# Performance work log

Measured on AMD Instinct MI355X. Metric: run time of the kernel, lower is better.

The kernel has to match this reference:

```python
import jax, jax.numpy as jnp
import numpy as np

N0, N1, N2 = 200000, 100000, 50000
E0, E1 = 1600000, 800000
IN_F, H_F, N_CLS = 128, 256, 64


def sage_conv(h_src, src_idx, dst_idx, num_dst, W_self, W_neigh, b):
    # DGL SAGEConv with aggregator_type='mean':
    #   h_neigh = mean over in-neighbors of h_src
    #   out = h_dst @ W_self + h_neigh @ W_neigh + b
    h_dst = h_src[:num_dst]
    msgs = h_src[src_idx]                                   # [E, F] gather
    summed = jax.ops.segment_sum(msgs, dst_idx, num_segments=num_dst)
    deg = jax.ops.segment_sum(jnp.ones((src_idx.shape[0],), h_src.dtype),
                              dst_idx, num_segments=num_dst)
    h_neigh = summed / jnp.maximum(deg, 1.0)[:, None]       # mean, safe for deg=0
    return h_dst @ W_self + h_neigh @ W_neigh + b


def setup_inputs() -> dict:
    key = jax.random.key(0)
    ks = jax.random.split(key, 10)
    s1 = 1.0 / np.sqrt(IN_F)
    s2 = 1.0 / np.sqrt(H_F)
    return {
        "x": jax.random.normal(ks[0], (N0, IN_F), jnp.float32),
        "src0": jax.random.randint(ks[1], (E0,), 0, N0, jnp.int64 if jax.config.jax_enable_x64 else jnp.int32),
        "dst0": jnp.sort(jax.random.randint(ks[2], (E0,), 0, N1)),
        "src1": jax.random.randint(ks[3], (E1,), 0, N1),
        "dst1": jnp.sort(jax.random.randint(ks[4], (E1,), 0, N2)),
        "num_dst0": N1,
        "num_dst1": N2,
        "W_self1": jax.random.normal(ks[5], (IN_F, H_F), jnp.float32) * s1,
        "W_neigh1": jax.random.normal(ks[6], (IN_F, H_F), jnp.float32) * s1,
        "b1": jnp.zeros((H_F,), jnp.float32),
        "W_self2": jax.random.normal(ks[7], (H_F, N_CLS), jnp.float32) * s2,
        "W_neigh2": jax.random.normal(ks[8], (H_F, N_CLS), jnp.float32) * s2,
        "b2": jnp.zeros((N_CLS,), jnp.float32),
    }


def reference(x, src0, dst0, src1, dst1, num_dst0, num_dst1,
              W_self1, W_neigh1, b1, W_self2, W_neigh2, b2):
    h = sage_conv(x, src0, dst0, num_dst0, W_self1, W_neigh1, b1)   # [N1, H]
    h = jax.nn.relu(h)
    h = sage_conv(h, src1, dst1, num_dst1, W_self2, W_neigh2, b2)   # [N2, C]
    return h
```

## Files before the change

kernel.cpp:

```cpp
#include <hip/hip_runtime.h>

constexpr int cN0  = 200000;
constexpr int cN1  = 100000;
constexpr int cN2  = 50000;
constexpr int cE0  = 1600000;
constexpr int cE1  = 800000;
constexpr int cIN  = 128;
constexpr int cH   = 256;
constexpr int cCLS = 64;

constexpr float QSTEP = 6.0f / 127.0f;
constexpr float QINV  = 127.0f / 6.0f;

using bf16x8 = __attribute__((ext_vector_type(8))) short;
using f32x4  = __attribute__((ext_vector_type(4))) float;

__device__ __forceinline__ float bflo(unsigned int u) {
    union { unsigned int i; float f; } v; v.i = u << 16; return v.f;
}
__device__ __forceinline__ float bfhi(unsigned int u) {
    union { unsigned int i; float f; } v; v.i = u & 0xFFFF0000u; return v.f;
}
__device__ __forceinline__ unsigned int f2bf(float f) {
    union { float f; unsigned int i; } v; v.f = f;
    return (v.i + 0x7FFFu + ((v.i >> 16) & 1u)) >> 16;
}

constexpr int PV   = 8;
constexpr int AF4  = cN1 * cIN / 4;
constexpr int ABLK = (AF4 + 256 * PV - 1) / (256 * PV);
constexpr int BF4  = (cN0 - cN1) * cIN / 4;
constexpr int BBLK = (BF4 + 256 * PV - 1) / (256 * PV);
constexpr int WCNT = cH * cH + 2 * cCLS * cH;
constexpr int WBLK = WCNT / 256;
constexpr int RCNT = (cN1 + 1) + (cN2 + 1);
constexpr int RBLK = (RCNT + 255) / 256;

__global__ __launch_bounds__(256) void prep(
        const float* __restrict__ x,
        const float* __restrict__ Ws1, const float* __restrict__ Wn1,
        const float* __restrict__ Wn2, const float* __restrict__ Ws2,
        const int* __restrict__ dst0, const int* __restrict__ dst1,
        unsigned short* __restrict__ xb, unsigned int* __restrict__ xq,
        unsigned short* __restrict__ Wt1, unsigned short* __restrict__ Wt2,
        int* __restrict__ row0, int* __restrict__ row1) {
    const int b = blockIdx.x, tid = threadIdx.x;
    if (b < ABLK + BBLK) {
        const bool hasXB = (b < ABLK);
        const int  lb    = hasXB ? b : b - ABLK;
        const int  limit = hasXB ? AF4 : BF4;
        const int  base  = lb * 256 * PV + tid;
        const float4* xp = (const float4*)x + (hasXB ? 0 : (size_t)AF4);
        const int  xqoff = hasXB ? 0 : AF4;

        float4 v[PV];
        #pragma unroll
        for (int j = 0; j < PV; ++j) {
            int idx = base + j * 256;
            int cidx = idx < limit ? idx : limit - 1;
            v[j] = xp[cidx];
        }
        auto q8b = [](float f) -> unsigned int {
            int q = __float2int_rn(f * QINV);
            q = q > 127 ? 127 : (q < -127 ? -127 : q);
            return (unsigned int)(q + 128);
        };
        #pragma unroll
        for (int j = 0; j < PV; ++j) {
            int idx = base + j * 256;
            if (idx >= limit) continue;
            float4 a = v[j];
            if (hasXB) {
                uint2 o;
                o.x = f2bf(a.x) | (f2bf(a.y) << 16);
                o.y = f2bf(a.z) | (f2bf(a.w) << 16);
                ((uint2*)xb)[idx] = o;
            }
            unsigned int d = q8b(a.x) | (q8b(a.y) << 8) |
                             (q8b(a.z) << 16) | (q8b(a.w) << 24);
            xq[xqoff + idx] = d;
        }
    } else if (b < ABLK + BBLK + WBLK) {
        const int wi = (b - ABLK - BBLK) * 256 + tid;
        if (wi < cH * cH) {
            int n = wi >> 8, k = wi & 255;
            float v = (k < cIN) ? Ws1[k * cH + n] : Wn1[(k - cIN) * cH + n];
            Wt1[n * cH + k] = (unsigned short)f2bf(v);
        } else {
            int j = wi - cH * cH; int n = j >> 8, k = j & 255;
            float v = (n < cCLS) ? Wn2[k * cCLS + n] : Ws2[k * cCLS + (n - cCLS)];
            Wt2[n * cH + k] = (unsigned short)f2bf(v);
        }
    } else {
        const int ti = (b - ABLK - BBLK - WBLK) * 256 + tid;
        if (ti <= cN1) {
            int lo = 0, hi = cE0;
            while (lo < hi) { int mid = (lo + hi) >> 1; if (dst0[mid] < ti) lo = mid + 1; else hi = mid; }
            row0[ti] = lo;
        } else {
            int d = ti - (cN1 + 1);
            if (d <= cN2) {
                int lo = 0, hi = cE1;
                while (lo < hi) { int mid = (lo + hi) >> 1; if (dst1[mid] < d) lo = mid + 1; else hi = mid; }
                row1[d] = lo;
            }
        }
    }
}

__global__ __launch_bounds__(256) void agg_i8(
        const uint2* __restrict__ xq,
        const int* __restrict__ sidx,
        const int* __restrict__ rows,
        unsigned short* __restrict__ nb,
        int num_dst) {
    const int tid = threadIdx.x, lane = tid & 63;
    const int m = blockIdx.x * 4 + (tid >> 6);
    if (m >= num_dst) return;
    const int sub = lane >> 4, t = lane & 15;
    const int e0 = rows[m], e1 = rows[m + 1];

    unsigned int accA = 0, accB = 0, accC = 0, accD = 0;
    auto addq = [&](uint2 v) {
        accA += v.x & 0x00FF00FFu;
        accB += (v.x >> 8) & 0x00FF00FFu;
        accC += v.y & 0x00FF00FFu;
        accD += (v.y >> 8) & 0x00FF00FFu;
    };

    int base = e0;
    for (; base + 16 <= e1; base += 16) {
        int sA = sidx[base + sub];
        int sB = sidx[base + 4 + sub];
        int sC = sidx[base + 8 + sub];
        int sD = sidx[base + 12 + sub];
        uint2 vA = xq[(size_t)sA * 16 + t];
        uint2 vB = xq[(size_t)sB * 16 + t];
        uint2 vC = xq[(size_t)sC * 16 + t];
        uint2 vD = xq[(size_t)sD * 16 + t];
        addq(vA); addq(vB); addq(vC); addq(vD);
    }
    for (; base < e1; base += 4) {
        int idx = base + sub;
        if (idx < e1) addq(xq[(size_t)sidx[idx] * 16 + t]);
    }

    accA += __shfl_xor((int)accA, 16, 64); accA += __shfl_xor((int)accA, 32, 64);
    accB += __shfl_xor((int)accB, 16, 64); accB += __shfl_xor((int)accB, 32, 64);
    accC += __shfl_xor((int)accC, 16, 64); accC += __shfl_xor((int)accC, 32, 64);
    accD += __shfl_xor((int)accD, 16, 64); accD += __shfl_xor((int)accD, 32, 64);

    if (sub == 0) {
        const int deg = e1 - e0;
        const float inv  = QSTEP / (float)(deg > 1 ? deg : 1);
        const float bias = 128.0f * (float)deg;
        auto cv = [&](unsigned int field) -> float {
            return ((float)(int)field - bias) * inv;
        };
        float f0 = cv(accA & 0xFFFFu), f2 = cv(accA >> 16);
        float f1 = cv(accB & 0xFFFFu), f3 = cv(accB >> 16);
        float f4 = cv(accC & 0xFFFFu), f6 = cv(accC >> 16);
        float f5 = cv(accD & 0xFFFFu), f7 = cv(accD >> 16);
        uint4 w;
        w.x = f2bf(f0) | (f2bf(f1) << 16);
        w.y = f2bf(f2) | (f2bf(f3) << 16);
        w.z = f2bf(f4) | (f2bf(f5) << 16);
        w.w = f2bf(f6) | (f2bf(f7) << 16);
        ((uint4*)nb)[(size_t)m * 16 + t] = w;
    }
}

template<int K, bool ACCUM>
__global__ __launch_bounds__(256) void agg_wave(
        const unsigned short* __restrict__ src,
        const int* __restrict__ sidx,
        const int* __restrict__ rows,
        void* __restrict__ outv, int num_dst) {
    constexpr int LPR = K / 8;
    constexpr int EPW = 64 / LPR;
    const int tid = threadIdx.x;
    const int lane = tid & 63;
    const int m = blockIdx.x * 4 + (tid >> 6);
    if (m >= num_dst) return;
    const int sub = lane / LPR;
    const int t   = lane % LPR;

    const uint4* s4 = (const uint4*)src;
    const int e0 = rows[m], e1 = rows[m + 1];

    float acc[8];
    #pragma unroll
    for (int j = 0; j < 8; ++j) acc[j] = 0.f;
    auto addv = [&](uint4 v) {
        acc[0] += bflo(v.x); acc[1] += bfhi(v.x);
        acc[2] += bflo(v.y); acc[3] += bfhi(v.y);
        acc[4] += bflo(v.z); acc[5] += bfhi(v.z);
        acc[6] += bflo(v.w); acc[7] += bfhi(v.w);
    };

    int base = e0;
    for (; base + 2 * EPW <= e1; base += 2 * EPW) {
        int sA = sidx[base + sub], sB = sidx[base + EPW + sub];
        uint4 vA = s4[(size_t)sA * LPR + t];
        uint4 vB = s4[(size_t)sB * LPR + t];
        addv(vA); addv(vB);
    }
    for (; base < e1; base += EPW) {
        int idx = base + sub;
        if (idx < e1) addv(s4[(size_t)sidx[idx] * LPR + t]);
    }

    #pragma unroll
    for (int j = 0; j < 8; ++j) {
        #pragma unroll
        for (int off = LPR; off < 64; off <<= 1)
            acc[j] += __shfl_xor(acc[j], off, 64);
    }

    if (sub == 0) {
        const int deg = e1 - e0;
        const float inv = 1.0f / (float)(deg > 1 ? deg : 1);
        if (!ACCUM) {
            uint4 o;
            o.x = f2bf(acc[0] * inv) | (f2bf(acc[1] * inv) << 16);
            o.y = f2bf(acc[2] * inv) | (f2bf(acc[3] * inv) << 16);
            o.z = f2bf(acc[4] * inv) | (f2bf(acc[5] * inv) << 16);
            o.w = f2bf(acc[6] * inv) | (f2bf(acc[7] * inv) << 16);
            ((uint4*)outv)[(size_t)m * LPR + t] = o;
        } else {
            float* op = (float*)outv + (size_t)m * K + t * 8;
            float4 o0 = *(float4*)op, o1 = *(float4*)(op + 4);
            o0.x += acc[0] * inv; o0.y += acc[1] * inv;
            o0.z += acc[2] * inv; o0.w += acc[3] * inv;
            o1.x += acc[4] * inv; o1.y += acc[5] * inv;
            o1.z += acc[6] * inv; o1.w += acc[7] * inv;
            *(float4*)op = o0; *(float4*)(op + 4) = o1;
        }
    }
}

template<int BM, int BN, int WM, int WN, bool RELU, bool HASBIAS, bool OUTBF16>
__global__ __launch_bounds__(256) void gemm_mfma(
        const unsigned short* __restrict__ A1, int K1,
        const unsigned short* __restrict__ A2, int K2,
        const unsigned short* __restrict__ Bt,
        const float* __restrict__ bias,
        void* __restrict__ Cout, int M, int N) {
    static_assert(2 * WM * 16 == BM && 2 * WN * 16 == BN, "wave tiling");
    __shared__ unsigned short As[BM][40];
    __shared__ unsigned short Bs[BN][40];

    const int tid = threadIdx.x;
    const int m0 = blockIdx.x * BM, n0 = blockIdx.y * BN;
    const int lane = tid & 63, wave = tid >> 6;
    const int wrow = wave >> 1, wcol = wave & 1;
    const int quad = lane >> 4, l16 = lane & 15;
    const int K = K1 + K2;

    f32x4 acc[WM][WN];
    #pragma unroll
    for (int i = 0; i < WM; ++i)
        #pragma unroll
        for (int j = 0; j < WN; ++j)
            acc[i][j] = (f32x4){0.f, 0.f, 0.f, 0.f};

    for (int kb = 0; kb < K; kb += 32) {
        const unsigned short* Ab; int lda, kloc;
        if (kb < K1) { Ab = A1; lda = K1; kloc = kb; }
        else         { Ab = A2; lda = K2; kloc = kb - K1; }

        #pragma unroll
        for (int f = 0; f < (BM * 4) / 256; ++f) {
            int idx = tid + f * 256;
            int row = idx >> 2, q = idx & 3;
            int gm = m0 + row;
            uint4 v = make_uint4(0, 0, 0, 0);
            if (gm < M) v = *(const uint4*)(Ab + (size_t)gm * lda + kloc + q * 8);
            *(uint4*)&As[row][q * 8] = v;
        }
        #pragma unroll
        for (int f = 0; f < (BN * 4) / 256; ++f) {
            int idx = tid + f * 256;
            int row = idx >> 2, q = idx & 3;
            uint4 v = *(const uint4*)(Bt + (size_t)(n0 + row) * K + kb + q * 8);
            *(uint4*)&Bs[row][q * 8] = v;
        }
        __syncthreads();

        bf16x8 a[WM], b[WN];
        #pragma unroll
        for (int i = 0; i < WM; ++i)
            a[i] = *(const bf16x8*)&As[(wrow * WM + i) * 16 + l16][quad * 8];
        #pragma unroll
        for (int j = 0; j < WN; ++j)
            b[j] = *(const bf16x8*)&Bs[(wcol * WN + j) * 16 + l16][quad * 8];
        #pragma unroll
        for (int i = 0; i < WM; ++i)
            #pragma unroll
            for (int j = 0; j < WN; ++j)
                acc[i][j] = __builtin_amdgcn_mfma_f32_16x16x32_bf16(
                    a[i], b[j], acc[i][j], 0, 0, 0);
        __syncthreads();
    }

    float bv[WN];
    #pragma unroll
    for (int j = 0; j < WN; ++j)
        bv[j] = HASBIAS ? bias[n0 + (wcol * WN + j) * 16 + l16] : 0.f;
    #pragma unroll
    for (int i = 0; i < WM; ++i) {
        #pragma unroll
        for (int r = 0; r < 4; ++r) {
            int gm = m0 + (wrow * WM + i) * 16 + quad * 4 + r;
            if (gm >= M) continue;
            #pragma unroll
            for (int j = 0; j < WN; ++j) {
                int gn = n0 + (wcol * WN + j) * 16 + l16;
                float v = acc[i][j][r] + bv[j];
                if (RELU) v = fmaxf(v, 0.f);
                if (OUTBF16)
                    ((unsigned short*)Cout)[(size_t)gm * N + gn] = (unsigned short)f2bf(v);
                else
                    ((float*)Cout)[(size_t)gm * N + gn] = v;
            }
        }
    }
}

__global__ __launch_bounds__(256) void gemm2_split(
        const unsigned short* __restrict__ A,
        const unsigned short* __restrict__ Bt,
        const float* __restrict__ b2,
        unsigned short* __restrict__ zb,
        float* __restrict__ out) {
    __shared__ unsigned short As[128][40];
    __shared__ unsigned short Bs[128][40];
    const int tid = threadIdx.x;
    const int m0 = blockIdx.x * 128;
    const int lane = tid & 63, wave = tid >> 6;
    const int wrow = wave >> 1, wcol = wave & 1;
    const int quad = lane >> 4, l16 = lane & 15;

    f32x4 acc[4][4];
    #pragma unroll
    for (int i = 0; i < 4; ++i)
        #pragma unroll
        for (int j = 0; j < 4; ++j)
            acc[i][j] = (f32x4){0.f, 0.f, 0.f, 0.f};

    for (int kb = 0; kb < cH; kb += 32) {
        #pragma unroll
        for (int f = 0; f < 2; ++f) {
            int idx = tid + f * 256;
            int row = idx >> 2, q = idx & 3;
            int gm = m0 + row;
            uint4 v = make_uint4(0, 0, 0, 0);
            if (gm < cN1) v = *(const uint4*)(A + (size_t)gm * cH + kb + q * 8);
            *(uint4*)&As[row][q * 8] = v;
        }
        #pragma unroll
        for (int f = 0; f < 2; ++f) {
            int idx = tid + f * 256;
            int row = idx >> 2, q = idx & 3;
            uint4 v = *(const uint4*)(Bt + (size_t)row * cH + kb + q * 8);
            *(uint4*)&Bs[row][q * 8] = v;
        }
        __syncthreads();

        bf16x8 a[4], b[4];
        #pragma unroll
        for (int i = 0; i < 4; ++i)
            a[i] = *(const bf16x8*)&As[(wrow * 4 + i) * 16 + l16][quad * 8];
        #pragma unroll
        for (int j = 0; j < 4; ++j)
            b[j] = *(const bf16x8*)&Bs[(wcol * 4 + j) * 16 + l16][quad * 8];
        #pragma unroll
        for (int i = 0; i < 4; ++i)
            #pragma unroll
            for (int j = 0; j < 4; ++j)
                acc[i][j] = __builtin_amdgcn_mfma_f32_16x16x32_bf16(
                    a[i], b[j], acc[i][j], 0, 0, 0);
        __syncthreads();
    }

    if (wcol == 0) {
        #pragma unroll
        for (int i = 0; i < 4; ++i) {
            #pragma unroll
            for (int r = 0; r < 4; ++r) {
                int gm = m0 + (wrow * 4 + i) * 16 + quad * 4 + r;
                if (gm >= cN1) continue;
                #pragma unroll
                for (int j = 0; j < 4; ++j) {
                    int gn = j * 16 + l16;
                    zb[(size_t)gm * cCLS + gn] = (unsigned short)f2bf(acc[i][j][r]);
                }
            }
        }
    } else {
        float bv[4];
        #pragma unroll
        for (int j = 0; j < 4; ++j) bv[j] = b2[j * 16 + l16];
        #pragma unroll
        for (int i = 0; i < 4; ++i) {
            #pragma unroll
            for (int r = 0; r < 4; ++r) {
                int gm = m0 + (wrow * 4 + i) * 16 + quad * 4 + r;
                if (gm >= cN2) continue;
                #pragma unroll
                for (int j = 0; j < 4; ++j)
                    out[(size_t)gm * cCLS + j * 16 + l16] = acc[i][j][r] + bv[j];
            }
        }
    }
}

extern "C" void kernel_launch(void* const* d_in, const int* in_sizes, int n_in,
                              void* d_out, int out_size, void* d_ws, size_t ws_size,
                              hipStream_t stream) {
    const float* x      = (const float*)d_in[0];
    const int*   src0   = (const int*)d_in[1];
    const int*   dst0   = (const int*)d_in[2];
    const int*   src1   = (const int*)d_in[3];
    const int*   dst1   = (const int*)d_in[4];
    const float* Wself1  = (const float*)d_in[7];
    const float* Wneigh1 = (const float*)d_in[8];
    const float* b1      = (const float*)d_in[9];
    const float* Wself2  = (const float*)d_in[10];
    const float* Wneigh2 = (const float*)d_in[11];
    const float* b2      = (const float*)d_in[12];
    float* out = (float*)d_out;

    char* ws = (char*)d_ws;
    int* row0 = (int*)ws;
    int* row1 = row0 + (cN1 + 1);
    size_t off = (size_t)((cN1 + 1) + (cN2 + 1)) * sizeof(int);
    off = (off + 1023) & ~(size_t)1023;
    unsigned short* xb = (unsigned short*)(ws + off); off += (size_t)cN1 * cIN * 2;
    unsigned int*   xq = (unsigned int*)(ws + off);
    unsigned short* zb = (unsigned short*)(ws + off); off += (size_t)cN0 * cIN;
    unsigned short* nb  = (unsigned short*)(ws + off); off += (size_t)cN1 * cIN * 2;
    unsigned short* h1b = (unsigned short*)(ws + off); off += (size_t)cN1 * cH * 2;
    unsigned short* Wt1 = (unsigned short*)(ws + off); off += (size_t)cH * cH * 2;
    unsigned short* Wt2 = (unsigned short*)(ws + off); off += (size_t)2 * cCLS * cH * 2;

    prep<<<ABLK + BBLK + WBLK + RBLK, 256, 0, stream>>>(
        x, Wself1, Wneigh1, Wneigh2, Wself2, dst0, dst1,
        xb, xq, Wt1, Wt2, row0, row1);

    agg_i8<<<(cN1 + 3) / 4, 256, 0, stream>>>(
        (const uint2*)xq, src0, row0, nb, cN1);

    gemm_mfma<128, 128, 4, 4, true, true, true>
        <<<dim3((cN1 + 127) / 128, cH / 128), 256, 0, stream>>>(
        xb, cIN, nb, cIN, Wt1, b1, h1b, cN1, cH);

    gemm2_split<<<(cN1 + 127) / 128, 256, 0, stream>>>(h1b, Wt2, b2, zb, out);

    agg_wave<cCLS, true><<<(cN2 + 3) / 4, 256, 0, stream>>>(
        zb, src1, row1, out, cN2);
}
```

Baseline: 335.0 us.

## Fuse fp32-to-bf16 conversion of x into layer-1 GEMM and widen tile to full N

The prep kernel no longer writes a bf16 copy of x. Instead, the layer-1 GEMM reads fp32 x directly and converts it to bf16 while staging tiles into shared memory. The GEMM becomes a 512-thread kernel that covers all 256 output columns per block, so the A tile is loaded once rather than once per N-half. The int8 aggregation loop is also merged into a single predicated 16-edge loop, which removes the separate tail loop. The trade-off is that the GEMM now reads fp32 x, twice the bytes of bf16, and has higher register and LDS pressure per block.

```diff
diff --git a/kernel.cpp b/kernel.cpp
--- a/kernel.cpp
+++ b/kernel.cpp
@@ -27,10 +27,8 @@
 }
 
 constexpr int PV   = 8;
-constexpr int AF4  = cN1 * cIN / 4;
-constexpr int ABLK = (AF4 + 256 * PV - 1) / (256 * PV);
-constexpr int BF4  = (cN0 - cN1) * cIN / 4;
-constexpr int BBLK = (BF4 + 256 * PV - 1) / (256 * PV);
+constexpr int QF4  = cN0 * cIN / 4;
+constexpr int QBLK = QF4 / (256 * PV);
 constexpr int WCNT = cH * cH + 2 * cCLS * cH;
 constexpr int WBLK = WCNT / 256;
 constexpr int RCNT = (cN1 + 1) + (cN2 + 1);
@@ -41,25 +39,18 @@
         const float* __restrict__ Ws1, const float* __restrict__ Wn1,
         const float* __restrict__ Wn2, const float* __restrict__ Ws2,
         const int* __restrict__ dst0, const int* __restrict__ dst1,
-        unsigned short* __restrict__ xb, unsigned int* __restrict__ xq,
+        unsigned int* __restrict__ xq,
         unsigned short* __restrict__ Wt1, unsigned short* __restrict__ Wt2,
         int* __restrict__ row0, int* __restrict__ row1) {
     const int b = blockIdx.x, tid = threadIdx.x;
-    if (b < ABLK + BBLK) {
-        const bool hasXB = (b < ABLK);
-        const int  lb    = hasXB ? b : b - ABLK;
-        const int  limit = hasXB ? AF4 : BF4;
-        const int  base  = lb * 256 * PV + tid;
-        const float4* xp = (const float4*)x + (hasXB ? 0 : (size_t)AF4);
-        const int  xqoff = hasXB ? 0 : AF4;
+    if (b < QBLK) {
+        const int base = b * 256 * PV + tid;
+        const float4* xp = (const float4*)x;
 
         float4 v[PV];
         #pragma unroll
-        for (int j = 0; j < PV; ++j) {
-            int idx = base + j * 256;
-            int cidx = idx < limit ? idx : limit - 1;
-            v[j] = xp[cidx];
-        }
+        for (int j = 0; j < PV; ++j)
+            v[j] = xp[base + j * 256];
         auto q8b = [](float f) -> unsigned int {
             int q = __float2int_rn(f * QINV);
             q = q > 127 ? 127 : (q < -127 ? -127 : q);
@@ -67,21 +58,13 @@
         };
         #pragma unroll
         for (int j = 0; j < PV; ++j) {
-            int idx = base + j * 256;
-            if (idx >= limit) continue;
             float4 a = v[j];
-            if (hasXB) {
-                uint2 o;
-                o.x = f2bf(a.x) | (f2bf(a.y) << 16);
-                o.y = f2bf(a.z) | (f2bf(a.w) << 16);
-                ((uint2*)xb)[idx] = o;
-            }
             unsigned int d = q8b(a.x) | (q8b(a.y) << 8) |
                              (q8b(a.z) << 16) | (q8b(a.w) << 24);
-            xq[xqoff + idx] = d;
-        }
-    } else if (b < ABLK + BBLK + WBLK) {
-        const int wi = (b - ABLK - BBLK) * 256 + tid;
+            xq[base + j * 256] = d;
+        }
+    } else if (b < QBLK + WBLK) {
+        const int wi = (b - QBLK) * 256 + tid;
         if (wi < cH * cH) {
             int n = wi >> 8, k = wi & 255;
             float v = (k < cIN) ? Ws1[k * cH + n] : Wn1[(k - cIN) * cH + n];
@@ -92,7 +75,7 @@
             Wt2[n * cH + k] = (unsigned short)f2bf(v);
         }
     } else {
-        const int ti = (b - ABLK - BBLK - WBLK) * 256 + tid;
+        const int ti = (b - QBLK - WBLK) * 256 + tid;
         if (ti <= cN1) {
             int lo = 0, hi = cE0;
             while (lo < hi) { int mid = (lo + hi) >> 1; if (dst0[mid] < ti) lo = mid + 1; else hi = mid; }
@@ -121,28 +104,27 @@
     const int e0 = rows[m], e1 = rows[m + 1];
 
     unsigned int accA = 0, accB = 0, accC = 0, accD = 0;
-    auto addq = [&](uint2 v) {
-        accA += v.x & 0x00FF00FFu;
-        accB += (v.x >> 8) & 0x00FF00FFu;
-        accC += v.y & 0x00FF00FFu;
-        accD += (v.y >> 8) & 0x00FF00FFu;
-    };
-
-    int base = e0;
-    for (; base + 16 <= e1; base += 16) {
-        int sA = sidx[base + sub];
-        int sB = sidx[base + 4 + sub];
-        int sC = sidx[base + 8 + sub];
-        int sD = sidx[base + 12 + sub];
-        uint2 vA = xq[(size_t)sA * 16 + t];
-        uint2 vB = xq[(size_t)sB * 16 + t];
-        uint2 vC = xq[(size_t)sC * 16 + t];
-        uint2 vD = xq[(size_t)sD * 16 + t];
-        addq(vA); addq(vB); addq(vC); addq(vD);
-    }
-    for (; base < e1; base += 4) {
-        int idx = base + sub;
-        if (idx < e1) addq(xq[(size_t)sidx[idx] * 16 + t]);
+
+    for (int base = e0; base < e1; base += 16) {
+        int s[4]; bool val[4];
+        #pragma unroll
+        for (int k = 0; k < 4; ++k) {
+            int ei = base + k * 4 + sub;
+            val[k] = ei < e1;
+            s[k] = sidx[val[k] ? ei : e0];
+        }
+        uint2 v[4];
+        #pragma unroll
+        for (int k = 0; k < 4; ++k)
+            v[k] = xq[(size_t)s[k] * 16 + t];
+        #pragma unroll
+        for (int k = 0; k < 4; ++k) {
+            uint2 w = val[k] ? v[k] : make_uint2(0u, 0u);
+            accA += w.x & 0x00FF00FFu;
+            accB += (w.x >> 8) & 0x00FF00FFu;
+            accC += w.y & 0x00FF00FFu;
+            accD += (w.y >> 8) & 0x00FF00FFu;
+        }
     }
 
     accA += __shfl_xor((int)accA, 16, 64); accA += __shfl_xor((int)accA, 32, 64);
@@ -239,89 +221,91 @@
     }
 }
 
-template<int BM, int BN, int WM, int WN, bool RELU, bool HASBIAS, bool OUTBF16>
-__global__ __launch_bounds__(256) void gemm_mfma(
-        const unsigned short* __restrict__ A1, int K1,
-        const unsigned short* __restrict__ A2, int K2,
+__global__ __launch_bounds__(512) void gemm1_fused(
+        const float* __restrict__ X,
+        const unsigned short* __restrict__ NB,
         const unsigned short* __restrict__ Bt,
         const float* __restrict__ bias,
-        void* __restrict__ Cout, int M, int N) {
-    static_assert(2 * WM * 16 == BM && 2 * WN * 16 == BN, "wave tiling");
-    __shared__ unsigned short As[BM][40];
-    __shared__ unsigned short Bs[BN][40];
+        unsigned short* __restrict__ C) {
+    __shared__ unsigned short As[128][40];
+    __shared__ unsigned short Bs[256][40];
 
     const int tid = threadIdx.x;
-    const int m0 = blockIdx.x * BM, n0 = blockIdx.y * BN;
+    const int m0 = blockIdx.x * 128;
     const int lane = tid & 63, wave = tid >> 6;
-    const int wrow = wave >> 1, wcol = wave & 1;
+    const int wrow = wave >> 2, wcol = wave & 3;
     const int quad = lane >> 4, l16 = lane & 15;
-    const int K = K1 + K2;
-
-    f32x4 acc[WM][WN];
-    #pragma unroll
-    for (int i = 0; i < WM; ++i)
-        #pragma unroll
-        for (int j = 0; j < WN; ++j)
+
+    f32x4 acc[4][4];
+    #pragma unroll
+    for (int i = 0; i < 4; ++i)
+        #pragma unroll
+        for (int j = 0; j < 4; ++j)
             acc[i][j] = (f32x4){0.f, 0.f, 0.f, 0.f};
 
-    for (int kb = 0; kb < K; kb += 32) {
-        const unsigned short* Ab; int lda, kloc;
-        if (kb < K1) { Ab = A1; lda = K1; kloc = kb; }
-        else         { Ab = A2; lda = K2; kloc = kb - K1; }
-
-        #pragma unroll
-        for (int f = 0; f < (BM * 4) / 256; ++f) {
-            int idx = tid + f * 256;
+    const int arow = tid >> 2, aq = tid & 3;
+    const int gma  = m0 + arow;
+
+    for (int kb = 0; kb < cH; kb += 32) {
+        if (kb < cIN) {
+            float4 a0 = {0,0,0,0}, a1 = {0,0,0,0};
+            if (gma < cN1) {
+                const float4* p = (const float4*)(X + (size_t)gma * cIN + kb + aq * 8);
+                a0 = p[0]; a1 = p[1];
+            }
+            uint4 v;
+            v.x = f2bf(a0.x) | (f2bf(a0.y) << 16);
+            v.y = f2bf(a0.z) | (f2bf(a0.w) << 16);
+            v.z = f2bf(a1.x) | (f2bf(a1.y) << 16);
+            v.w = f2bf(a1.z) | (f2bf(a1.w) << 16);
+            *(uint4*)&As[arow][aq * 8] = v;
+        } else {
+            uint4 v = make_uint4(0, 0, 0, 0);
+            if (gma < cN1)
+                v = *(const uint4*)(NB + (size_t)gma * cIN + (kb - cIN) + aq * 8);
+            *(uint4*)&As[arow][aq * 8] = v;
+        }
+        #pragma unroll
+        for (int f = 0; f < 2; ++f) {
+            int idx = tid + f * 512;
             int row = idx >> 2, q = idx & 3;
-            int gm = m0 + row;
-            uint4 v = make_uint4(0, 0, 0, 0);
-            if (gm < M) v = *(const uint4*)(Ab + (size_t)gm * lda + kloc + q * 8);
-            *(uint4*)&As[row][q * 8] = v;
-        }
-        #pragma unroll
-        for (int f = 0; f < (BN * 4) / 256; ++f) {
-            int idx = tid + f * 256;
-            int row = idx >> 2, q = idx & 3;
-            uint4 v = *(const uint4*)(Bt + (size_t)(n0 + row) * K + kb + q * 8);
+            uint4 v = *(const uint4*)(Bt + (size_t)row * cH + kb + q * 8);
             *(uint4*)&Bs[row][q * 8] = v;
         }
         __syncthreads();
 
-        bf16x8 a[WM], b[WN];
-        #pragma unroll
-        for (int i = 0; i < WM; ++i)
-            a[i] = *(const bf16x8*)&As[(wrow * WM + i) * 16 + l16][quad * 8];
-        #pragma unroll
-        for (int j = 0; j < WN; ++j)
-            b[j] = *(const bf16x8*)&Bs[(wcol * WN + j) * 16 + l16][quad * 8];
-        #pragma unroll
-        for (int i = 0; i < WM; ++i)
+        bf16x8 a[4], b[4];
+        #pragma unroll
+        for (int i = 0; i < 4; ++i)
+            a[i] = *(const bf16x8*)&As[wrow * 64 + i * 16 + l16][quad * 8];
+        #pragma unroll
+        for (int j = 0; j < 4; ++j)
+            b[j] = *(const bf16x8*)&Bs[wcol * 64 + j * 16 + l16][quad * 8];
+        #pragma unroll
+        for (int i = 0; i < 4; ++i)
             #pragma unroll
-            for (int j = 0; j < WN; ++j)
+            for (int j = 0; j < 4; ++j)
                 acc[i][j] = __builtin_amdgcn_mfma_f32_16x16x32_bf16(
                     a[i], b[j], acc[i][j], 0, 0, 0);
         __syncthreads();
     }
 
-    float bv[WN];
-    #pragma unroll
-    for (int j = 0; j < WN; ++j)
-        bv[j] = HASBIAS ? bias[n0 + (wcol * WN + j) * 16 + l16] : 0.f;
-    #pragma unroll
-    for (int i = 0; i < WM; ++i) {
+    float bv[4];
+    #pragma unroll
+    for (int j = 0; j < 4; ++j)
+        bv[j] = bias[wcol * 64 + j * 16 + l16];
+    #pragma unroll
+    for (int i = 0; i < 4; ++i) {
         #pragma unroll
         for (int r = 0; r < 4; ++r) {
-            int gm = m0 + (wrow * WM + i) * 16 + quad * 4 + r;
-            if (gm >= M) continue;
+            int gm = m0 + wrow * 64 + i * 16 + quad * 4 + r;
+            if (gm >= cN1) continue;
             #pragma unroll
-            for (int j = 0; j < WN; ++j) {
-                int gn = n0 + (wcol * WN + j) * 16 + l16;
+            for (int j = 0; j < 4; ++j) {
+                int gn = wcol * 64 + j * 16 + l16;
                 float v = acc[i][j][r] + bv[j];
-                if (RELU) v = fmaxf(v, 0.f);
-                if (OUTBF16)
-                    ((unsigned short*)Cout)[(size_t)gm * N + gn] = (unsigned short)f2bf(v);
-                else
-                    ((float*)Cout)[(size_t)gm * N + gn] = v;
+                v = fmaxf(v, 0.f);
+                C[(size_t)gm * cH + gn] = (unsigned short)f2bf(v);
             }
         }
     }
@@ -436,7 +420,6 @@
     int* row1 = row0 + (cN1 + 1);
     size_t off = (size_t)((cN1 + 1) + (cN2 + 1)) * sizeof(int);
     off = (off + 1023) & ~(size_t)1023;
-    unsigned short* xb = (unsigned short*)(ws + off); off += (size_t)cN1 * cIN * 2;
     unsigned int*   xq = (unsigned int*)(ws + off);
     unsigned short* zb = (unsigned short*)(ws + off); off += (size_t)cN0 * cIN;
     unsigned short* nb  = (unsigned short*)(ws + off); off += (size_t)cN1 * cIN * 2;
@@ -444,16 +427,15 @@
     unsigned short* Wt1 = (unsigned short*)(ws + off); off += (size_t)cH * cH * 2;
     unsigned short* Wt2 = (unsigned short*)(ws + off); off += (size_t)2 * cCLS * cH * 2;
 
-    prep<<<ABLK + BBLK + WBLK + RBLK, 256, 0, stream>>>(
+    prep<<<QBLK + WBLK + RBLK, 256, 0, stream>>>(
         x, Wself1, Wneigh1, Wneigh2, Wself2, dst0, dst1,
-        xb, xq, Wt1, Wt2, row0, row1);
+        xq, Wt1, Wt2, row0, row1);
 
     agg_i8<<<(cN1 + 3) / 4, 256, 0, stream>>>(
         (const uint2*)xq, src0, row0, nb, cN1);
 
-    gemm_mfma<128, 128, 4, 4, true, true, true>
-        <<<dim3((cN1 + 127) / 128, cH / 128), 256, 0, stream>>>(
-        xb, cIN, nb, cIN, Wt1, b1, h1b, cN1, cH);
+    gemm1_fused<<<(cN1 + 127) / 128, 512, 0, stream>>>(
+        x, nb, Wt1, b1, h1b);
 
     gemm2_split<<<(cN1 + 127) / 128, 256, 0, stream>>>(h1b, Wt2, b2, zb, out);
 
```

Result: no change. 331.4 us (-1.1%).
